# Optimization experiments

Measured on AMD Instinct MI355X. Metric: run time of the kernel, lower is better.

## Reference

```python
import jax, jax.numpy as jnp
from jax import lax
import numpy as np

OUT_CH = 16      # texture_features
INTER = 32       # texture_features_intermediate
TEXDIM = 1024    # texture_dimensions
IN_SIZE = 76


def _leaky(x):
    return jnp.where(x >= 0, x, 0.02 * x)


def grid_sample_bilinear_border(tex, grid):
    """torch.nn.functional.grid_sample, mode='bilinear', padding_mode='border',
    align_corners=False.  tex: (N,C,H,W); grid: (N,Ho,Wo,2) with (x,y) in [-1,1].
    N == 1 here; vectorized over H,W via fancy indexing."""
    N, C, H, W = tex.shape
    x, y = grid[..., 0], grid[..., 1]
    # unnormalize (align_corners=False)
    ix = ((x + 1.0) * W - 1.0) * 0.5
    iy = ((y + 1.0) * H - 1.0) * 0.5
    # border padding: clamp continuous coords
    ix = jnp.clip(ix, 0.0, W - 1.0)
    iy = jnp.clip(iy, 0.0, H - 1.0)
    x0 = jnp.floor(ix); y0 = jnp.floor(iy)
    wx = ix - x0; wy = iy - y0
    x0i = jnp.clip(x0, 0, W - 1).astype(jnp.int32)
    x1i = jnp.clip(x0 + 1, 0, W - 1).astype(jnp.int32)
    y0i = jnp.clip(y0, 0, H - 1).astype(jnp.int32)
    y1i = jnp.clip(y0 + 1, 0, H - 1).astype(jnp.int32)
    t = tex[0]  # (C,H,W)
    v00 = t[:, y0i[0], x0i[0]]  # (C,Ho,Wo)
    v01 = t[:, y0i[0], x1i[0]]
    v10 = t[:, y1i[0], x0i[0]]
    v11 = t[:, y1i[0], x1i[0]]
    wx = wx[0][None]; wy = wy[0][None]  # (1,Ho,Wo) broadcast over C
    out = (v00 * (1 - wx) * (1 - wy) + v01 * wx * (1 - wy)
           + v10 * (1 - wx) * wy + v11 * wx * wy)
    return out[None]  # (1,C,Ho,Wo)


def setup_inputs() -> dict:
    key = jax.random.key(0)
    ks = jax.random.split(key, 11)
    expressions = jax.random.normal(ks[0], (1, IN_SIZE), jnp.float32)
    audio_features = jax.random.normal(ks[1], (1, 16), jnp.float32)
    uv_inputs = jax.random.uniform(ks[2], (1, 2, 1024, 1024), jnp.float32, -1.0, 1.0)
    data = jax.random.normal(ks[3], (1, INTER, TEXDIM, TEXDIM), jnp.float32)
    def lin(kw, kb, fo, fi):
        s = 1.0 / np.sqrt(fi).astype(np.float32)
        return (jax.random.uniform(kw, (fo, fi), jnp.float32, -s, s),
                jax.random.uniform(kb, (fo,), jnp.float32, -s, s))
    W1, b1 = lin(ks[4], ks[5], 128, IN_SIZE)
    W2, b2 = lin(ks[6], ks[7], 64, 128)
    W3, b3 = lin(ks[8], ks[9], OUT_CH * 4 * 4 * INTER, 64)
    return {"expressions": expressions, "audio_features": audio_features,
            "uv_inputs": uv_inputs, "data": data,
            "W1": W1, "b1": b1, "W2": W2, "b2": b2, "W3": W3, "b3": b3}


def reference(expressions, audio_features, uv_inputs, data, W1, b1, W2, b2, W3, b3):
    # tiny MLP -> dynamic 4x4 conv filter
    h = expressions.reshape(1, 1, -1)
    h = _leaky(h @ W1.T + b1)
    h = _leaky(h @ W2.T + b2)
    f = jnp.tanh(h @ W3.T + b3)
    conv_filter = f.reshape(OUT_CH, INTER, 4, 4)
    # conv2d(data, filter, stride=1, padding=2) -> (1, OUT_CH, D+1, D+1)
    tex_eval = lax.conv_general_dilated(
        data, conv_filter, window_strides=(1, 1), padding=((2, 2), (2, 2)),
        dimension_numbers=("NCHW", "OIHW", "NCHW"))
    # grid: stack x (chan 0) and y (chan 1) along last dim
    grid = jnp.stack([uv_inputs[:, 0], uv_inputs[:, 1]], axis=3)  # (1,Ho,Wo,2)
    return grid_sample_bilinear_border(tex_eval, grid)
```

## Files before the change

### kernel.cpp

```cpp
#include <hip/hip_runtime.h>
#include <math.h>

#define NPX   1048576
#define TD    1025
#define PW    35
#define PH    11
#define DPAD  1028
#define ROWB  65792
#define DP_OFF 33673216

typedef _Float16 half8 __attribute__((ext_vector_type(8)));
typedef _Float16 half4 __attribute__((ext_vector_type(4)));
typedef float    f32x4 __attribute__((ext_vector_type(4)));

__device__ __forceinline__ void load_lds16(const void* g, void* lds) {
    __builtin_amdgcn_global_load_lds(
        (const __attribute__((address_space(1))) void*)g,
        (__attribute__((address_space(3))) void*)lds, 16, 0, 0);
}

__global__ __launch_bounds__(256) void mlp_kernel(
    const float* __restrict__ expr,
    const float* __restrict__ W1, const float* __restrict__ b1,
    const float* __restrict__ W2, const float* __restrict__ b2,
    const float* __restrict__ W3, const float* __restrict__ b3,
    _Float16* __restrict__ ffrag_g)
{
    __shared__ float sx[76];
    __shared__ float sh1[128];
    __shared__ float sh2[64];
    int t = threadIdx.x;
    if (t < 76) sx[t] = expr[t];
    __syncthreads();
    if (t < 128) {
        float a = b1[t];
        const float* w = W1 + t * 76;
        #pragma unroll 4
        for (int i = 0; i < 76; ++i) a += sx[i] * w[i];
        sh1[t] = a >= 0.f ? a : 0.02f * a;
    }
    __syncthreads();
    if (t < 64) {
        float a = b2[t];
        const float* w = W2 + t * 128;
        #pragma unroll 4
        for (int i = 0; i < 128; ++i) a += sh1[i] * w[i];
        sh2[t] = a >= 0.f ? a : 0.02f * a;
    }
    __syncthreads();
    int o = blockIdx.x * 256 + t;
    float a = b3[o];
    const float* w = W3 + o * 64;
    #pragma unroll 4
    for (int i = 0; i < 64; ++i) a += sh2[i] * w[i];
    a = tanhf(a);
    int oc = o >> 9;
    int ic = (o >> 4) & 31;
    int kk = o & 15;
    ffrag_g[(size_t)(kk * 64 + (ic >> 3) * 16 + oc) * 8 + (ic & 7)] = (_Float16)a;
}

__global__ __launch_bounds__(256) void repack_kernel(
    const float* __restrict__ data, _Float16* __restrict__ Dp)
{
    __shared__ _Float16 s[256 * 32];
    int tid = threadIdx.x;
    int Y = blockIdx.y;
    int X = blockIdx.x * 256 + tid;
    int y = Y - 2, x = X - 2;
    bool ok = ((unsigned)y < 1024u) && ((unsigned)x < 1024u);
    const float* dp = data + ((size_t)y << 10) + x;

    float v[32];
    #pragma unroll
    for (int j = 0; j < 32; ++j) v[j] = 0.f;
    if (ok) {
        #pragma unroll
        for (int j = 0; j < 32; ++j) v[j] = __builtin_nontemporal_load(&dp[(size_t)j * NPX]);
    }
    #pragma unroll
    for (int g = 0; g < 4; ++g) {
        half8 h;
        #pragma unroll
        for (int j = 0; j < 8; ++j) h[j] = (_Float16)v[g * 8 + j];
        int chunk = tid * 4 + g;
        int sw = chunk ^ ((chunk >> 3) & 7);
        *(half8*)((char*)s + sw * 16) = h;
    }
    __syncthreads();
    char* rowbase = (char*)Dp + (size_t)Y * ROWB + blockIdx.x * 16384;
    int lim = ROWB - blockIdx.x * 16384;
    #pragma unroll
    for (int i = 0; i < 4; ++i) {
        int off = tid * 16 + i * 4096;
        if (off < lim) {
            int chunk = tid + i * 256;
            int sw = chunk ^ ((chunk >> 3) & 7);
            *(uint4*)(rowbase + off) = *(uint4*)((char*)s + sw * 16);
        }
    }
}

__global__ __launch_bounds__(256, 4) void conv_mfma_kernel(
    const _Float16* __restrict__ Dp,
    const _Float16* __restrict__ ffrag_g,
    _Float16* __restrict__ tex)
{
    __shared__ __attribute__((aligned(128))) _Float16 sp[PH * PW * 32];

    int tid = threadIdx.x;
    int l = tid & 63, w = tid >> 6;
    int ox0 = blockIdx.x * 32;
    int oy0 = blockIdx.y * 8;

    half8 bfrag[16];
    #pragma unroll
    for (int kk = 0; kk < 16; ++kk)
        bfrag[kk] = *(const half8*)&ffrag_g[kk * 512 + l * 8];

    int lsw = l ^ ((l >> 3) & 7);
    for (int r = w; r < PH; r += 4) {
        int gy = min(oy0 + r, DPAD - 1);
        const char* grow = (const char*)Dp + (size_t)gy * ROWB;
        _Float16* lrow = sp + r * (PW * 32);
        #pragma unroll
        for (int c = 0; c < 3; ++c) {
            int off = ox0 * 64 + c * 1024 + lsw * 16;
            off = min(off, ROWB - 16);
            if (c < 2 || l < 12)
                load_lds16(grow + off, (char*)lrow + c * 1024);
        }
    }
    __syncthreads();

    int lane15 = l & 15;
    int q = l >> 4;

    int u = lane15 * 4 + q;
    int sv[4];
    #pragma unroll
    for (int kx = 0; kx < 4; ++kx) {
        int vch = kx * 4 + u;
        sv[kx] = (vch ^ ((vch >> 3) & 7)) * 16;
    }

    f32x4 acc[4];
    #pragma unroll
    for (int t = 0; t < 4; ++t) acc[t] = (f32x4){0.f, 0.f, 0.f, 0.f};

    #pragma unroll
    for (int kk = 0; kk < 16; ++kk) {
        int ky = kk >> 2, kx = kk & 3;
        #pragma unroll
        for (int t = 0; t < 4; ++t) {
            const char* ap = (const char*)sp
                + (w * 2 + (t >> 1) + ky) * (PW * 64)
                + (t & 1) * 1024 + sv[kx];
            half8 af = *(const half8*)ap;
            acc[t] = __builtin_amdgcn_mfma_f32_16x16x32_f16(bfrag[kk], af, acc[t], 0, 0, 0);
        }
    }

    #pragma unroll
    for (int t = 0; t < 4; ++t) {
        int oy = oy0 + w * 2 + (t >> 1);
        int px = ox0 + (t & 1) * 16 + lane15;
        if (oy > 1024 || px > 1024) continue;
        half4 hv;
        #pragma unroll
        for (int r = 0; r < 4; ++r) hv[r] = (_Float16)acc[t][r];
        *(half4*)&tex[((size_t)oy * TD + px) * 16 + q * 4] = hv;
    }
}

__global__ __launch_bounds__(256, 6) void sample_kernel(
    const float* __restrict__ uv,
    const _Float16* __restrict__ tex,
    float* __restrict__ out)
{
    int p = blockIdx.x * 256 + threadIdx.x;
    float x = __builtin_nontemporal_load(&uv[p]);
    float y = __builtin_nontemporal_load(&uv[NPX + p]);
    float ix = fminf(fmaxf(((x + 1.f) * 1025.f - 1.f) * 0.5f, 0.f), 1024.f);
    float iy = fminf(fmaxf(((y + 1.f) * 1025.f - 1.f) * 0.5f, 0.f), 1024.f);
    float fx0 = floorf(ix), fy0 = floorf(iy);
    float wx = ix - fx0, wy = iy - fy0;
    int x0 = (int)fx0, y0 = (int)fy0;
    int x1 = min(x0 + 1, 1024), y1 = min(y0 + 1, 1024);

    const half8* t00 = (const half8*)(tex + ((size_t)y0 * TD + x0) * 16);
    const half8* t01 = (const half8*)(tex + ((size_t)y0 * TD + x1) * 16);
    const half8* t10 = (const half8*)(tex + ((size_t)y1 * TD + x0) * 16);
    const half8* t11 = (const half8*)(tex + ((size_t)y1 * TD + x1) * 16);

    half8 v0 = t00[0], v1 = t00[1];
    half8 v2 = t01[0], v3 = t01[1];
    half8 v4 = t10[0], v5 = t10[1];
    half8 v6 = t11[0], v7 = t11[1];

    float w00 = (1.f - wx) * (1.f - wy);
    float w01 = wx * (1.f - wy);
    float w10 = (1.f - wx) * wy;
    float w11 = wx * wy;

    #pragma unroll
    for (int c = 0; c < 8; ++c) {
        float r0 = (float)v0[c] * w00 + (float)v2[c] * w01
                 + (float)v4[c] * w10 + (float)v6[c] * w11;
        float r1 = (float)v1[c] * w00 + (float)v3[c] * w01
                 + (float)v5[c] * w10 + (float)v7[c] * w11;
        __builtin_nontemporal_store(r0, &out[(size_t)c * NPX + p]);
        __builtin_nontemporal_store(r1, &out[(size_t)(c + 8) * NPX + p]);
    }
}

extern "C" void kernel_launch(void* const* d_in, const int* in_sizes, int n_in,
                              void* d_out, int out_size, void* d_ws, size_t ws_size,
                              hipStream_t stream) {
    const float* expr = (const float*)d_in[0];
    const float* uv   = (const float*)d_in[2];
    const float* data = (const float*)d_in[3];
    const float* W1   = (const float*)d_in[4];
    const float* b1   = (const float*)d_in[5];
    const float* W2   = (const float*)d_in[6];
    const float* b2   = (const float*)d_in[7];
    const float* W3   = (const float*)d_in[8];
    const float* b3   = (const float*)d_in[9];
    float* out = (float*)d_out;

    _Float16* ffrag_g  = (_Float16*)d_ws;
    _Float16* tex      = (_Float16*)((char*)d_ws + 49152);
    _Float16* Dp       = (_Float16*)((char*)d_ws + DP_OFF);

    mlp_kernel<<<32, 256, 0, stream>>>(expr, W1, b1, W2, b2, W3, b3, ffrag_g);
    repack_kernel<<<dim3(5, DPAD), 256, 0, stream>>>(data, Dp);
    conv_mfma_kernel<<<dim3(33, 129), 256, 0, stream>>>(Dp, ffrag_g, tex);
    sample_kernel<<<NPX / 256, 256, 0, stream>>>(uv, tex, out);
}
```

Measured before the change: 326.5 us.

## Fuse fp32-to-fp16 repack into conv kernel tile load

Removes the separate repack kernel that converted and padded the input into an fp16 channel-interleaved buffer. The conv kernel now loads fp32 data directly from global memory, zero-fills the borders, converts to fp16 and scatters it into the swizzled LDS tile. This avoids writing and rereading the intermediate buffer and drops one launch. The cost is reading fp32 halos redundantly across blocks and doing scalar 2-byte LDS stores instead of async 16-byte LDS loads.

```diff
diff --git a/kernel.cpp b/kernel.cpp
--- a/kernel.cpp
+++ b/kernel.cpp
@@ -5,19 +5,10 @@
 #define TD    1025
 #define PW    35
 #define PH    11
-#define DPAD  1028
-#define ROWB  65792
-#define DP_OFF 33673216
 
 typedef _Float16 half8 __attribute__((ext_vector_type(8)));
 typedef _Float16 half4 __attribute__((ext_vector_type(4)));
 typedef float    f32x4 __attribute__((ext_vector_type(4)));
-
-__device__ __forceinline__ void load_lds16(const void* g, void* lds) {
-    __builtin_amdgcn_global_load_lds(
-        (const __attribute__((address_space(1))) void*)g,
-        (__attribute__((address_space(3))) void*)lds, 16, 0, 0);
-}
 
 __global__ __launch_bounds__(256) void mlp_kernel(
     const float* __restrict__ expr,
@@ -60,49 +51,8 @@
     ffrag_g[(size_t)(kk * 64 + (ic >> 3) * 16 + oc) * 8 + (ic & 7)] = (_Float16)a;
 }
 
-__global__ __launch_bounds__(256) void repack_kernel(
-    const float* __restrict__ data, _Float16* __restrict__ Dp)
-{
-    __shared__ _Float16 s[256 * 32];
-    int tid = threadIdx.x;
-    int Y = blockIdx.y;
-    int X = blockIdx.x * 256 + tid;
-    int y = Y - 2, x = X - 2;
-    bool ok = ((unsigned)y < 1024u) && ((unsigned)x < 1024u);
-    const float* dp = data + ((size_t)y << 10) + x;
-
-    float v[32];
-    #pragma unroll
-    for (int j = 0; j < 32; ++j) v[j] = 0.f;
-    if (ok) {
-        #pragma unroll
-        for (int j = 0; j < 32; ++j) v[j] = __builtin_nontemporal_load(&dp[(size_t)j * NPX]);
-    }
-    #pragma unroll
-    for (int g = 0; g < 4; ++g) {
-        half8 h;
-        #pragma unroll
-        for (int j = 0; j < 8; ++j) h[j] = (_Float16)v[g * 8 + j];
-        int chunk = tid * 4 + g;
-        int sw = chunk ^ ((chunk >> 3) & 7);
-        *(half8*)((char*)s + sw * 16) = h;
-    }
-    __syncthreads();
-    char* rowbase = (char*)Dp + (size_t)Y * ROWB + blockIdx.x * 16384;
-    int lim = ROWB - blockIdx.x * 16384;
-    #pragma unroll
-    for (int i = 0; i < 4; ++i) {
-        int off = tid * 16 + i * 4096;
-        if (off < lim) {
-            int chunk = tid + i * 256;
-            int sw = chunk ^ ((chunk >> 3) & 7);
-            *(uint4*)(rowbase + off) = *(uint4*)((char*)s + sw * 16);
-        }
-    }
-}
-
 __global__ __launch_bounds__(256, 4) void conv_mfma_kernel(
-    const _Float16* __restrict__ Dp,
+    const float* __restrict__ data,
     const _Float16* __restrict__ ffrag_g,
     _Float16* __restrict__ tex)
 {
@@ -118,17 +68,38 @@
     for (int kk = 0; kk < 16; ++kk)
         bfrag[kk] = *(const half8*)&ffrag_g[kk * 512 + l * 8];
 
-    int lsw = l ^ ((l >> 3) & 7);
-    for (int r = w; r < PH; r += 4) {
-        int gy = min(oy0 + r, DPAD - 1);
-        const char* grow = (const char*)Dp + (size_t)gy * ROWB;
-        _Float16* lrow = sp + r * (PW * 32);
-        #pragma unroll
-        for (int c = 0; c < 3; ++c) {
-            int off = ox0 * 64 + c * 1024 + lsw * 16;
-            off = min(off, ROWB - 16);
-            if (c < 2 || l < 12)
-                load_lds16(grow + off, (char*)lrow + c * 1024);
+    for (int r = 0; r < PH; ++r) {
+        int gy = oy0 + r - 2;
+        bool rowok = ((unsigned)gy < 1024u);
+        const float* drow = data + (size_t)gy * 1024;
+        char* lrow = (char*)sp + r * 2240;
+        int nit = (tid < 64) ? 2 : 1;
+        for (int it = 0; it < nit; ++it) {
+            int idx = tid + it * 256;
+            int c = idx / 10;
+            int xg = idx - c * 10;
+            int gx = (ox0 - 4) + xg * 4;
+            f32x4 v = (f32x4){0.f, 0.f, 0.f, 0.f};
+            if (rowok) {
+                const float* src = drow + (size_t)c * NPX + gx;
+                if ((unsigned)gx <= 1020u) {
+                    v = *(const f32x4*)src;
+                } else {
+                    #pragma unroll
+                    for (int k = 0; k < 4; ++k)
+                        if ((unsigned)(gx + k) < 1024u) v[k] = src[k];
+                }
+            }
+            int q8 = c >> 3, c7 = (c & 7) * 2;
+            #pragma unroll
+            for (int k = 0; k < 4; ++k) {
+                int xL = xg * 4 + k - 2;
+                if ((unsigned)xL < 35u) {
+                    int chunk = xL * 4 + q8;
+                    int swc = chunk ^ ((chunk >> 3) & 7);
+                    *(_Float16*)(lrow + swc * 16 + c7) = (_Float16)v[k];
+                }
+            }
         }
     }
     __syncthreads();
@@ -230,10 +201,8 @@
 
     _Float16* ffrag_g  = (_Float16*)d_ws;
     _Float16* tex      = (_Float16*)((char*)d_ws + 49152);
-    _Float16* Dp       = (_Float16*)((char*)d_ws + DP_OFF);
 
     mlp_kernel<<<32, 256, 0, stream>>>(expr, W1, b1, W2, b2, W3, b3, ffrag_g);
-    repack_kernel<<<dim3(5, DPAD), 256, 0, stream>>>(data, Dp);
-    conv_mfma_kernel<<<dim3(33, 129), 256, 0, stream>>>(Dp, ffrag_g, tex);
+    conv_mfma_kernel<<<dim3(33, 129), 256, 0, stream>>>(data, ffrag_g, tex);
     sample_kernel<<<NPX / 256, 256, 0, stream>>>(uv, tex, out);
 }
```

New measurement: 365.3 us. 1.12x slower.
